# Performance work log

Hardware: AMD Instinct MI355X
Metric: run time of the kernel (lower is better)

## Reference

```python
import jax, jax.numpy as jnp
import numpy as np

B, S, H = 8, 2048, 1024
NEG = 1.0e10


def setup_inputs() -> dict:
    key = jax.random.key(0)
    ks = jax.random.split(key, 9)
    scale = 1.0 / np.sqrt(H)
    x = jax.random.normal(ks[0], (B, S, H), dtype=jnp.float32)
    Wq = jax.random.normal(ks[1], (H, H), dtype=jnp.float32) * scale
    bq = jnp.zeros((H,), dtype=jnp.float32)
    Wk = jax.random.normal(ks[2], (H, H), dtype=jnp.float32) * scale
    bk = jnp.zeros((H,), dtype=jnp.float32)
    Wv = jax.random.normal(ks[3], (H, H), dtype=jnp.float32) * scale
    bv = jnp.zeros((H,), dtype=jnp.float32)
    gamma = jnp.ones((H,), dtype=jnp.float32)
    beta = jnp.zeros((H,), dtype=jnp.float32)
    return {"x": x, "Wq": Wq, "bq": bq, "Wk": Wk, "bk": bk,
            "Wv": Wv, "bv": bv, "gamma": gamma, "beta": beta}


def _layernorm(y, gamma, beta, eps=1e-5):
    mu = jnp.mean(y, axis=-1, keepdims=True)
    var = jnp.var(y, axis=-1, keepdims=True)
    return (y - mu) * jax.lax.rsqrt(var + eps) * gamma + beta


def reference(x, Wq, bq, Wk, bk, Wv, bv, gamma, beta):
    # QKV projections (single head, no 1/sqrt(d) scaling, per original code)
    q = x @ Wq + bq                       # [B, S, H]
    k = x @ Wk + bk                       # [B, S, H]
    v = x @ Wv + bv                       # [B, S, H]
    scores = jnp.einsum('bsh,bth->bst', q, k)   # [B, S, S]
    # non-standard multiplicative-subtractive causal mask
    mask = jnp.tril(jnp.ones((S, S), dtype=scores.dtype))  # [S, S]
    scores = scores * mask - NEG * (1.0 - mask)
    probs = jax.nn.softmax(scores, axis=-1)
    attn = jnp.einsum('bst,bth->bsh', probs, v)
    return _layernorm(v + attn, gamma, beta)
```

## Files before the change

### kernel.cpp

```cpp
#include <hip/hip_runtime.h>

#define SQ 2048
#define HD 1024
#define NB 8
#define NT2 8
#define NTOT (NB*SQ)
#define CE ((long long)72*32768)

typedef _Float16 f16x8 __attribute__((ext_vector_type(8)));
typedef float f32x4 __attribute__((ext_vector_type(4)));
typedef short s16x8 __attribute__((ext_vector_type(8)));
typedef short s16x4 __attribute__((ext_vector_type(4)));
typedef unsigned short u16;

__device__ __forceinline__ u16 f2h(float x){
  _Float16 h = (_Float16)x;
  u16 u; __builtin_memcpy(&u, &h, 2); return u;
}

__device__ __forceinline__ int TB128(int i){
  int m = i >> 1;
  return (i & 1) ? (m + 1) * (m + 1) : m * m + m;
}

#define STG(gp, lp) __builtin_amdgcn_global_load_lds( \
    (const __attribute__((address_space(1))) unsigned*)(gp), \
    (__attribute__((address_space(3))) unsigned*)(lp), 16, 0, 0)

template<int EPI>
__global__ __launch_bounds__(512, 2)
void gemm8(const u16* __restrict__ A, const u16* __restrict__ B,
           float* Cf, u16* Ch, u16* Vt,
           const float* __restrict__ b0, const float* __restrict__ b1,
           const float* __restrict__ b2,
           int K, int lda, int ldb, int ldc,
           long long sA, long long sB, long long sC)
{
  const int z = blockIdx.z;
  const int bi = blockIdx.x, bj = blockIdx.y;

  __shared__ short lds[65536];

  const int tid  = threadIdx.x;
  const int lane = tid & 63, w = tid >> 6;
  const int wm2 = w >> 2, wn4 = w & 3;
  const int lrow = lane & 15, kgrp = lane >> 4;

  const long long rowA = (long long)bi * 256;
  const long long colB = (long long)bj * 256;

  const int rt = tid >> 3;
  const int gs = (tid & 7) ^ (rt & 7);

  const u16 *sAp[4], *sBp[4];
  if (EPI == 2){
    const u16* P0 = A + (long long)z * sA + (long long)(bi * bi + bi) * 65536;
    const u16* P1 = A + (long long)z * sA + (long long)((bi + 1) * (bi + 1)) * 65536;
    sAp[0] = P0 + (      rt) * 512 + gs * 8;
    sAp[1] = P0 + (64  + rt) * 512 + gs * 8;
    sAp[2] = P1 + (      rt) * 512 + gs * 8;
    sAp[3] = P1 + (64  + rt) * 512 + gs * 8;
  } else {
    const u16* Ab0 = A;
    #pragma unroll
    for (int i = 0; i < 4; i++)
      sAp[i] = Ab0 + (rowA + i * 64 + rt) * (long long)lda + gs * 8;
  }
  {
    const u16* Bb = B + (long long)z * sB;
    #pragma unroll
    for (int i = 0; i < 4; i++)
      sBp[i] = Bb + (colB + i * 64 + rt) * (long long)ldb + gs * 8;
  }

  #define ADST(buf,i) (lds + (buf) * 32768 +         (i) * 4096 + w * 512)
  #define BDST(buf,i) (lds + (buf) * 32768 + 16384 + (i) * 4096 + w * 512)

  const int fl = lrow & 7;
  const int swzk[2] = { ((0 + kgrp) ^ fl) * 8, ((4 + kgrp) ^ fl) * 8 };
  const int arow = (wm2 * 128 + lrow) * 64;
  const int brow = 16384 + (wn4 * 64 + lrow) * 64;

  f32x4 acc[8][4];
  const f32x4 zf = {0.f, 0.f, 0.f, 0.f};
  #pragma unroll
  for (int m = 0; m < 8; m++)
    #pragma unroll
    for (int n = 0; n < 4; n++) acc[m][n] = zf;

  int KT = K >> 6;
  if (EPI == 2){ int t = (bi + 1) * 4; if (t < KT) KT = t; }

  auto advance = [&](int tS){
    long long advA = 64;
    if (EPI == 2) advA = ((tS & 3) == 3) ? (65536 - 192) : 64;
    #pragma unroll
    for (int i = 0; i < 4; i++){ sAp[i] += advA; sBp[i] += 64; }
  };

  #pragma unroll
  for (int i = 0; i < 4; i++) STG(sAp[i], ADST(0, i));
  #pragma unroll
  for (int i = 0; i < 4; i++) STG(sBp[i], BDST(0, i));
  advance(0);
  __syncthreads();

  int cur = 0;
  for (int kt = 0; kt < KT; ++kt){
    const bool pf = (kt + 1 < KT);
    const short* Ab = lds + cur * 32768;
    const int nb = cur ^ 1;

    if (pf){
      #pragma unroll
      for (int i = 0; i < 4; i++) STG(sAp[i], ADST(nb, i));
      #pragma unroll
      for (int i = 0; i < 4; i++) STG(sBp[i], BDST(nb, i));
      advance(kt + 1);
    }

    f16x8 bq[4][2];
    #pragma unroll
    for (int n = 0; n < 4; n++)
      #pragma unroll
      for (int ks = 0; ks < 2; ks++)
        bq[n][ks] = *(const f16x8*)(Ab + brow + n * 1024 + swzk[ks]);

    #pragma unroll
    for (int qm = 0; qm < 2; qm++){
      f16x8 aq[4][2];
      #pragma unroll
      for (int m4 = 0; m4 < 4; m4++)
        #pragma unroll
        for (int ks = 0; ks < 2; ks++)
          aq[m4][ks] = *(const f16x8*)(Ab + arow + (qm * 4 + m4) * 1024 + swzk[ks]);

      __builtin_amdgcn_s_setprio(1);
      #pragma unroll
      for (int ks = 0; ks < 2; ks++)
        #pragma unroll
        for (int n = 0; n < 4; n++)
          #pragma unroll
          for (int m4 = 0; m4 < 4; m4++)
            acc[qm * 4 + m4][n] =
              __builtin_amdgcn_mfma_f32_16x16x32_f16(aq[m4][ks], bq[n][ks],
                                                     acc[qm * 4 + m4][n], 0, 0, 0);
      __builtin_amdgcn_s_setprio(0);
    }

    __syncthreads();
    cur ^= 1;
  }
  #undef ADST
  #undef BDST

  if (EPI == 0){
    if (z < 2){
      u16* c = Ch + (long long)z * sC;
      const float* bias = z ? b1 : b0;
      #pragma unroll
      for (int n = 0; n < 4; n++){
        int col = (int)colB + wn4 * 64 + n * 16 + lrow;
        float ba = bias[col];
        #pragma unroll
        for (int m = 0; m < 8; m++){
          long long r = rowA + wm2 * 128 + m * 16 + kgrp * 4;
          #pragma unroll
          for (int j = 0; j < 4; j++)
            c[(r + j) * ldc + col] = f2h(acc[m][n][j] + ba);
        }
      }
    } else {
      #pragma unroll
      for (int n = 0; n < 4; n++){
        int col = (int)colB + wn4 * 64 + n * 16 + lrow;
        float ba = b2[col];
        #pragma unroll
        for (int m = 0; m < 8; m++){
          long long r = rowA + wm2 * 128 + m * 16 + kgrp * 4;
          int bb = (int)(r >> 11);
          int s  = (int)(r & 2047);
          u16* vtc = Vt + ((long long)bb * HD + col) * SQ + s;
          #pragma unroll
          for (int j = 0; j < 4; j++){
            float v = acc[m][n][j] + ba;
            Cf[(r + j) * ldc + col] = v;
            vtc[j] = f2h(v);
          }
        }
      }
    }
  } else {
    float* cf = Cf + (long long)z * sC;
    #pragma unroll
    for (int n = 0; n < 4; n++){
      int col = (int)colB + wn4 * 64 + n * 16 + lrow;
      #pragma unroll
      for (int m = 0; m < 8; m++){
        long long r = rowA + wm2 * 128 + m * 16 + kgrp * 4;
        #pragma unroll
        for (int j = 0; j < 4; j++){
          long long o = (r + j) * ldc + col;
          cf[o] = acc[m][n][j] + cf[o];
        }
      }
    }
  }
}

__global__ __launch_bounds__(512, 2)
void gemm_sc(const u16* __restrict__ A, const u16* __restrict__ B,
             float* Cf, long long sA, long long sB, long long sC)
{
  const int z = blockIdx.z;
  int t = blockIdx.x;
  int i = (int)(2.f * sqrtf((float)t));
  if (i > 15) i = 15;
  while (TB128(i + 1) <= t) ++i;
  while (TB128(i) > t) --i;
  const int bj = t - TB128(i);

  __shared__ short lds[2 * 24576];

  const int tid  = threadIdx.x;
  const int lane = tid & 63, w = tid >> 6;
  const int wm2 = w >> 2, wn4 = w & 3;
  const int lrow = lane & 15, kgrp = lane >> 4;

  const long long rowA = (long long)i * 128;
  const long long colB = (long long)bj * 256;

  const int rt = tid >> 3;
  const int gs = (tid & 7) ^ (rt & 7);

  const u16 *sAp[2], *sBp[4];
  {
    const u16* Ab0 = A + (long long)z * sA;
    #pragma unroll
    for (int k = 0; k < 2; k++)
      sAp[k] = Ab0 + (rowA + k * 64 + rt) * (long long)HD + gs * 8;
    const u16* Bb = B + (long long)z * sB;
    #pragma unroll
    for (int k = 0; k < 4; k++)
      sBp[k] = Bb + (colB + k * 64 + rt) * (long long)HD + gs * 8;
  }

  #define ADST2(buf,k) (lds + (buf) * 24576 +        (k) * 4096 + w * 512)
  #define BDST2(buf,k) (lds + (buf) * 24576 + 8192 + (k) * 4096 + w * 512)

  const int fl = lrow & 7;
  const int swzk[2] = { ((0 + kgrp) ^ fl) * 8, ((4 + kgrp) ^ fl) * 8 };
  const int arow = (wm2 * 64 + lrow) * 64;
  const int brow = 8192 + (wn4 * 64 + lrow) * 64;

  f32x4 acc[4][4];
  const f32x4 zf = {0.f, 0.f, 0.f, 0.f};
  #pragma unroll
  for (int m = 0; m < 4; m++)
    #pragma unroll
    for (int n = 0; n < 4; n++) acc[m][n] = zf;

  const int KT = HD >> 6;

  auto advance = [&](){
    #pragma unroll
    for (int k = 0; k < 2; k++) sAp[k] += 64;
    #pragma unroll
    for (int k = 0; k < 4; k++) sBp[k] += 64;
  };

  #pragma unroll
  for (int k = 0; k < 2; k++) STG(sAp[k], ADST2(0, k));
  #pragma unroll
  for (int k = 0; k < 4; k++) STG(sBp[k], BDST2(0, k));
  advance();
  __syncthreads();

  int cur = 0;
  for (int kt = 0; kt < KT; ++kt){
    const bool pf = (kt + 1 < KT);
    const short* Ab = lds + cur * 24576;
    const int nb = cur ^ 1;

    if (pf){
      #pragma unroll
      for (int k = 0; k < 2; k++) STG(sAp[k], ADST2(nb, k));
      #pragma unroll
      for (int k = 0; k < 4; k++) STG(sBp[k], BDST2(nb, k));
      advance();
    }

    f16x8 bq[4][2], aq[4][2];
    #pragma unroll
    for (int n = 0; n < 4; n++)
      #pragma unroll
      for (int ks = 0; ks < 2; ks++)
        bq[n][ks] = *(const f16x8*)(Ab + brow + n * 1024 + swzk[ks]);
    #pragma unroll
    for (int m = 0; m < 4; m++)
      #pragma unroll
      for (int ks = 0; ks < 2; ks++)
        aq[m][ks] = *(const f16x8*)(Ab + arow + m * 1024 + swzk[ks]);

    __builtin_amdgcn_s_setprio(1);
    #pragma unroll
    for (int ks = 0; ks < 2; ks++)
      #pragma unroll
      for (int n = 0; n < 4; n++)
        #pragma unroll
        for (int m = 0; m < 4; m++)
          acc[m][n] = __builtin_amdgcn_mfma_f32_16x16x32_f16(aq[m][ks], bq[n][ks],
                                                             acc[m][n], 0, 0, 0);
    __builtin_amdgcn_s_setprio(0);

    __syncthreads();
    cur ^= 1;
  }
  #undef ADST2
  #undef BDST2

  float* cf = Cf + (long long)z * sC + (long long)t * 32768;
  #pragma unroll
  for (int n = 0; n < 4; n++){
    int col = wn4 * 64 + n * 16 + lrow;
    #pragma unroll
    for (int m = 0; m < 4; m++){
      int r = wm2 * 64 + m * 16 + kgrp * 4;
      #pragma unroll
      for (int j = 0; j < 4; j++)
        cf[(r + j) * 256 + col] = acc[m][n][j];
    }
  }
}

__global__ __launch_bounds__(256)
void prep_x(const float* __restrict__ X, u16* __restrict__ Xh)
{
  const long long n8 = (long long)NTOT * HD / 8;
  for (long long i = (long long)blockIdx.x * 256 + threadIdx.x; i < n8;
       i += (long long)gridDim.x * 256){
    const float* p = X + i * 8;
    float4 a = *(const float4*)p;
    float4 b = *(const float4*)(p + 4);
    float f[8] = {a.x, a.y, a.z, a.w, b.x, b.y, b.z, b.w};
    s16x8 h;
    #pragma unroll
    for (int j = 0; j < 8; j++) h[j] = (short)f2h(f[j]);
    *(s16x8*)&Xh[i * 8] = h;
  }
}

__global__ void prep_w(const float* __restrict__ Wq, const float* __restrict__ Wk,
                       const float* __restrict__ Wv, u16* __restrict__ Wt)
{
  __shared__ float t[32][33];
  const float* Win = (blockIdx.z == 0) ? Wq : (blockIdx.z == 1) ? Wk : Wv;
  const size_t zo = (size_t)blockIdx.z * HD * HD;
  int n0 = blockIdx.x * 32, k0 = blockIdx.y * 32;
  int tx = threadIdx.x, ty = threadIdx.y;
  #pragma unroll
  for (int i = 0; i < 4; i++)
    t[ty + 8*i][tx] = Win[(size_t)(k0 + ty + 8*i) * HD + n0 + tx];
  __syncthreads();
  #pragma unroll
  for (int i = 0; i < 4; i++)
    Wt[zo + (size_t)(n0 + ty + 8*i) * HD + k0 + tx] = f2h(t[tx][ty + 8*i]);
}

__global__ __launch_bounds__(256)
void softmax_causal(const float* __restrict__ SC, u16* __restrict__ P)
{
  const int s = blockIdx.x;
  const int ti = s >> 7;
  const int tb = TB128(ti);
  const float* scb = SC + (long long)blockIdx.y * CE + (long long)tb * 32768
                   + (long long)(s & 127) * 256;
  u16* pb = P + (long long)blockIdx.y * (2 * CE) + (long long)tb * 65536
          + (long long)(s & 127) * 512;

  __shared__ float buf[SQ];
  __shared__ float red[4];
  const int tid = threadIdx.x, lane = tid & 63, wid = tid >> 6;

  float m = -3.4e38f;
  const int nfull = (s + 1) & ~3;
  for (int t4 = tid * 4; t4 < nfull; t4 += 1024){
    float4 v = *(const float4*)&scb[(t4 >> 8) * 32768 + (t4 & 255)];
    *(float4*)&buf[t4] = v;
    m = fmaxf(fmaxf(fmaxf(m, v.x), v.y), fmaxf(v.z, v.w));
  }
  for (int t = nfull + tid; t <= s; t += 256){
    float v = scb[(t >> 8) * 32768 + (t & 255)];
    buf[t] = v; m = fmaxf(m, v);
  }
  #pragma unroll
  for (int o = 32; o; o >>= 1) m = fmaxf(m, __shfl_xor(m, o));
  if (lane == 0) red[wid] = m;
  __syncthreads();
  m = fmaxf(fmaxf(red[0], red[1]), fmaxf(red[2], red[3]));
  __syncthreads();

  float sum = 0.f;
  for (int t = tid; t <= s; t += 256){ float e = __expf(buf[t] - m); buf[t] = e; sum += e; }
  #pragma unroll
  for (int o = 32; o; o >>= 1) sum += __shfl_xor(sum, o);
  if (lane == 0) red[wid] = sum;
  __syncthreads();
  sum = red[0] + red[1] + red[2] + red[3];
  const float inv = 1.f / sum;

  const int lim = ((ti >> 1) + 1) << 8;
  for (int t4 = tid * 4; t4 < lim; t4 += 1024){
    s16x4 pk;
    #pragma unroll
    for (int j = 0; j < 4; j++){
      int t = t4 + j;
      pk[j] = (t <= s) ? (short)f2h(buf[t] * inv) : (short)0;
    }
    *(s16x4*)&pb[(t4 >> 8) * 65536 + (t4 & 255)] = pk;
  }
}

__global__ __launch_bounds__(256)
void layernorm_inplace(float* __restrict__ Y, const float* __restrict__ gamma,
                       const float* __restrict__ beta)
{
  float* y = Y + (long long)blockIdx.x * HD;
  const int tid = threadIdx.x, lane = tid & 63, wid = tid >> 6;
  float xv[4];
  float s = 0.f, ss = 0.f;
  #pragma unroll
  for (int i = 0; i < 4; i++){
    float v = y[tid + i * 256];
    xv[i] = v; s += v; ss += v * v;
  }
  #pragma unroll
  for (int o = 32; o; o >>= 1){ s += __shfl_xor(s, o); ss += __shfl_xor(ss, o); }
  __shared__ float r1[4], r2[4];
  if (lane == 0){ r1[wid] = s; r2[wid] = ss; }
  __syncthreads();
  s  = r1[0] + r1[1] + r1[2] + r1[3];
  ss = r2[0] + r2[1] + r2[2] + r2[3];
  const float mu   = s * (1.f / HD);
  const float var  = ss * (1.f / HD) - mu * mu;
  const float rstd = rsqrtf(var + 1e-5f);
  #pragma unroll
  for (int i = 0; i < 4; i++){
    int c = tid + i * 256;
    y[c] = (xv[i] - mu) * rstd * gamma[c] + beta[c];
  }
}

extern "C" void kernel_launch(void* const* d_in, const int* in_sizes, int n_in,
                              void* d_out, int out_size, void* d_ws, size_t ws_size,
                              hipStream_t stream)
{
  const float* x     = (const float*)d_in[0];
  const float* Wq    = (const float*)d_in[1];
  const float* bq    = (const float*)d_in[2];
  const float* Wk    = (const float*)d_in[3];
  const float* bk    = (const float*)d_in[4];
  const float* Wv    = (const float*)d_in[5];
  const float* bv    = (const float*)d_in[6];
  const float* gamma = (const float*)d_in[7];
  const float* beta  = (const float*)d_in[8];
  float* out = (float*)d_out;

  char* wsp = (char*)d_ws;
  size_t off = 0;
  auto alloc = [&](size_t bytes) -> char* {
    char* p = wsp + off;
    off = (off + bytes + 255) & ~(size_t)255;
    return p;
  };

  u16* Wt = (u16*)alloc(3ULL * HD * HD * 2);
  u16* QK = (u16*)alloc(2ULL * NTOT * HD * 2);
  u16* Vt = (u16*)alloc((size_t)NB * HD * SQ * 2);

  size_t rem = (ws_size > off) ? (ws_size - off) : 0;
  size_t perb = (size_t)CE * 4;
  int G = (int)(rem / perb);
  if (G > NB) G = NB;
  if (G < 1)  G = 1;
  u16*   xh = (u16*)(wsp + off);
  float* SC = (float*)(wsp + off);

  u16* Qh = QK;
  u16* Kh = QK + (size_t)NTOT * HD;
  float* V = out;

  prep_x<<<dim3(2048), dim3(256), 0, stream>>>(x, xh);
  prep_w<<<dim3(HD/32, HD/32, 3), dim3(32, 8), 0, stream>>>(Wq, Wk, Wv, Wt);

  gemm8<0><<<dim3(NTOT/256, HD/256, 3), 512, 0, stream>>>(
      xh, Wt, V, QK, Vt, bq, bk, bv,
      HD, HD, HD, HD,
      0LL, (long long)HD * HD, (long long)NTOT * HD);

  for (int g0 = 0; g0 < NB; g0 += G){
    int g = (G < NB - g0) ? G : (NB - g0);
    gemm_sc<<<dim3(72, 1, g), 512, 0, stream>>>(
        Qh + (size_t)g0 * SQ * HD, Kh + (size_t)g0 * SQ * HD, SC,
        (long long)SQ * HD, (long long)SQ * HD, CE);
    softmax_causal<<<dim3(SQ, g), 256, 0, stream>>>(SC, (u16*)SC);
    gemm8<2><<<dim3(NT2, HD/256, g), 512, 0, stream>>>(
        (const u16*)SC, Vt + (size_t)g0 * HD * SQ,
        out + (size_t)g0 * SQ * HD, nullptr, nullptr, nullptr, nullptr, nullptr,
        SQ, 512, SQ, HD,
        2 * CE, (long long)HD * SQ, (long long)SQ * HD);
  }

  layernorm_inplace<<<dim3(NTOT), 256, 0, stream>>>(out, gamma, beta);
}
```

Measured before the change: 332.9 us.

## Split causal PV GEMM into dedicated 128-row-tile kernel for better load balance

Measured after the change: 333.4 us. No clear change (+0.2%).

```diff
diff --git a/kernel.cpp b/kernel.cpp
--- a/kernel.cpp
+++ b/kernel.cpp
@@ -53,14 +53,7 @@
   const int gs = (tid & 7) ^ (rt & 7);
 
   const u16 *sAp[4], *sBp[4];
-  if (EPI == 2){
-    const u16* P0 = A + (long long)z * sA + (long long)(bi * bi + bi) * 65536;
-    const u16* P1 = A + (long long)z * sA + (long long)((bi + 1) * (bi + 1)) * 65536;
-    sAp[0] = P0 + (      rt) * 512 + gs * 8;
-    sAp[1] = P0 + (64  + rt) * 512 + gs * 8;
-    sAp[2] = P1 + (      rt) * 512 + gs * 8;
-    sAp[3] = P1 + (64  + rt) * 512 + gs * 8;
-  } else {
+  {
     const u16* Ab0 = A;
     #pragma unroll
     for (int i = 0; i < 4; i++)
@@ -88,21 +81,18 @@
     #pragma unroll
     for (int n = 0; n < 4; n++) acc[m][n] = zf;
 
-  int KT = K >> 6;
-  if (EPI == 2){ int t = (bi + 1) * 4; if (t < KT) KT = t; }
-
-  auto advance = [&](int tS){
-    long long advA = 64;
-    if (EPI == 2) advA = ((tS & 3) == 3) ? (65536 - 192) : 64;
-    #pragma unroll
-    for (int i = 0; i < 4; i++){ sAp[i] += advA; sBp[i] += 64; }
+  const int KT = K >> 6;
+
+  auto advance = [&](){
+    #pragma unroll
+    for (int i = 0; i < 4; i++){ sAp[i] += 64; sBp[i] += 64; }
   };
 
   #pragma unroll
   for (int i = 0; i < 4; i++) STG(sAp[i], ADST(0, i));
   #pragma unroll
   for (int i = 0; i < 4; i++) STG(sBp[i], BDST(0, i));
-  advance(0);
+  advance();
   __syncthreads();
 
   int cur = 0;
@@ -116,7 +106,7 @@
       for (int i = 0; i < 4; i++) STG(sAp[i], ADST(nb, i));
       #pragma unroll
       for (int i = 0; i < 4; i++) STG(sBp[i], BDST(nb, i));
-      advance(kt + 1);
+      advance();
     }
 
     f16x8 bq[4][2];
@@ -154,54 +144,37 @@
   #undef ADST
   #undef BDST
 
-  if (EPI == 0){
-    if (z < 2){
-      u16* c = Ch + (long long)z * sC;
-      const float* bias = z ? b1 : b0;
-      #pragma unroll
-      for (int n = 0; n < 4; n++){
-        int col = (int)colB + wn4 * 64 + n * 16 + lrow;
-        float ba = bias[col];
-        #pragma unroll
-        for (int m = 0; m < 8; m++){
-          long long r = rowA + wm2 * 128 + m * 16 + kgrp * 4;
-          #pragma unroll
-          for (int j = 0; j < 4; j++)
-            c[(r + j) * ldc + col] = f2h(acc[m][n][j] + ba);
-        }
-      }
-    } else {
-      #pragma unroll
-      for (int n = 0; n < 4; n++){
-        int col = (int)colB + wn4 * 64 + n * 16 + lrow;
-        float ba = b2[col];
-        #pragma unroll
-        for (int m = 0; m < 8; m++){
-          long long r = rowA + wm2 * 128 + m * 16 + kgrp * 4;
-          int bb = (int)(r >> 11);
-          int s  = (int)(r & 2047);
-          u16* vtc = Vt + ((long long)bb * HD + col) * SQ + s;
-          #pragma unroll
-          for (int j = 0; j < 4; j++){
-            float v = acc[m][n][j] + ba;
-            Cf[(r + j) * ldc + col] = v;
-            vtc[j] = f2h(v);
-          }
-        }
-      }
-    }
-  } else {
-    float* cf = Cf + (long long)z * sC;
+  if (z < 2){
+    u16* c = Ch + (long long)z * sC;
+    const float* bias = z ? b1 : b0;
     #pragma unroll
     for (int n = 0; n < 4; n++){
       int col = (int)colB + wn4 * 64 + n * 16 + lrow;
+      float ba = bias[col];
       #pragma unroll
       for (int m = 0; m < 8; m++){
         long long r = rowA + wm2 * 128 + m * 16 + kgrp * 4;
         #pragma unroll
+        for (int j = 0; j < 4; j++)
+          c[(r + j) * ldc + col] = f2h(acc[m][n][j] + ba);
+      }
+    }
+  } else {
+    #pragma unroll
+    for (int n = 0; n < 4; n++){
+      int col = (int)colB + wn4 * 64 + n * 16 + lrow;
+      float ba = b2[col];
+      #pragma unroll
+      for (int m = 0; m < 8; m++){
+        long long r = rowA + wm2 * 128 + m * 16 + kgrp * 4;
+        int bb = (int)(r >> 11);
+        int s  = (int)(r & 2047);
+        u16* vtc = Vt + ((long long)bb * HD + col) * SQ + s;
+        #pragma unroll
         for (int j = 0; j < 4; j++){
-          long long o = (r + j) * ldc + col;
-          cf[o] = acc[m][n][j] + cf[o];
+          float v = acc[m][n][j] + ba;
+          Cf[(r + j) * ldc + col] = v;
+          vtc[j] = f2h(v);
         }
       }
     }
@@ -329,6 +302,131 @@
       #pragma unroll
       for (int j = 0; j < 4; j++)
         cf[(r + j) * 256 + col] = acc[m][n][j];
+    }
+  }
+}
+
+__global__ __launch_bounds__(512, 2)
+void gemm_pv(const u16* __restrict__ P, const u16* __restrict__ Vt,
+             float* __restrict__ Out,
+             long long sP, long long sVt, long long sO)
+{
+  const int z = blockIdx.z;
+  const int ti = 15 - (int)blockIdx.x;
+  const int bj = blockIdx.y;
+  const int tb = TB128(ti);
+
+  __shared__ short lds[2 * 24576];
+
+  const int tid  = threadIdx.x;
+  const int lane = tid & 63, w = tid >> 6;
+  const int wm2 = w >> 2, wn4 = w & 3;
+  const int lrow = lane & 15, kgrp = lane >> 4;
+
+  const long long rowA = (long long)ti * 128;
+  const long long colB = (long long)bj * 256;
+
+  const int rt = tid >> 3;
+  const int gs = (tid & 7) ^ (rt & 7);
+
+  const u16 *sAp[2], *sBp[4];
+  {
+    const u16* Pb = P + (long long)z * sP + (long long)tb * 65536;
+    #pragma unroll
+    for (int k = 0; k < 2; k++)
+      sAp[k] = Pb + (k * 64 + rt) * 512 + gs * 8;
+    const u16* Bb = Vt + (long long)z * sVt;
+    #pragma unroll
+    for (int k = 0; k < 4; k++)
+      sBp[k] = Bb + (colB + k * 64 + rt) * (long long)SQ + gs * 8;
+  }
+
+  #define ADST3(buf,k) (lds + (buf) * 24576 +        (k) * 4096 + w * 512)
+  #define BDST3(buf,k) (lds + (buf) * 24576 + 8192 + (k) * 4096 + w * 512)
+
+  const int fl = lrow & 7;
+  const int swzk[2] = { ((0 + kgrp) ^ fl) * 8, ((4 + kgrp) ^ fl) * 8 };
+  const int arow = (wm2 * 64 + lrow) * 64;
+  const int brow = 8192 + (wn4 * 64 + lrow) * 64;
+
+  f32x4 acc[4][4];
+  const f32x4 zf = {0.f, 0.f, 0.f, 0.f};
+  #pragma unroll
+  for (int m = 0; m < 4; m++)
+    #pragma unroll
+    for (int n = 0; n < 4; n++) acc[m][n] = zf;
+
+  const int KT = ((ti >> 1) + 1) * 4;
+
+  auto advance = [&](int tS){
+    long long advA = ((tS & 3) == 3) ? (65536 - 192) : 64;
+    sAp[0] += advA; sAp[1] += advA;
+    #pragma unroll
+    for (int k = 0; k < 4; k++) sBp[k] += 64;
+  };
+
+  #pragma unroll
+  for (int k = 0; k < 2; k++) STG(sAp[k], ADST3(0, k));
+  #pragma unroll
+  for (int k = 0; k < 4; k++) STG(sBp[k], BDST3(0, k));
+  advance(0);
+  __syncthreads();
+
+  int cur = 0;
+  for (int kt = 0; kt < KT; ++kt){
+    const bool pf = (kt + 1 < KT);
+    const short* Ab = lds + cur * 24576;
+    const int nb = cur ^ 1;
+
+    if (pf){
+      #pragma unroll
+      for (int k = 0; k < 2; k++) STG(sAp[k], ADST3(nb, k));
+      #pragma unroll
+      for (int k = 0; k < 4; k++) STG(sBp[k], BDST3(nb, k));
+      advance(kt + 1);
+    }
+
+    f16x8 bq[4][2], aq[4][2];
+    #pragma unroll
+    for (int n = 0; n < 4; n++)
+      #pragma unroll
+      for (int ks = 0; ks < 2; ks++)
+        bq[n][ks] = *(const f16x8*)(Ab + brow + n * 1024 + swzk[ks]);
+    #pragma unroll
+    for (int m = 0; m < 4; m++)
+      #pragma unroll
+      for (int ks = 0; ks < 2; ks++)
+        aq[m][ks] = *(const f16x8*)(Ab + arow + m * 1024 + swzk[ks]);
+
+    __builtin_amdgcn_s_setprio(1);
+    #pragma unroll
+    for (int ks = 0; ks < 2; ks++)
+      #pragma unroll
+      for (int n = 0; n < 4; n++)
+        #pragma unroll
+        for (int m = 0; m < 4; m++)
+          acc[m][n] = __builtin_amdgcn_mfma_f32_16x16x32_f16(aq[m][ks], bq[n][ks],
+                                                             acc[m][n], 0, 0, 0);
+    __builtin_amdgcn_s_setprio(0);
+
+    __syncthreads();
+    cur ^= 1;
+  }
+  #undef ADST3
+  #undef BDST3
+
+  float* of = Out + (long long)z * sO;
+  #pragma unroll
+  for (int n = 0; n < 4; n++){
+    int col = (int)colB + wn4 * 64 + n * 16 + lrow;
+    #pragma unroll
+    for (int m = 0; m < 4; m++){
+      long long r = rowA + wm2 * 64 + m * 16 + kgrp * 4;
+      #pragma unroll
+      for (int j = 0; j < 4; j++){
+        long long o = (r + j) * HD + col;
+        of[o] = acc[m][n][j] + of[o];
+      }
     }
   }
 }
@@ -504,10 +602,9 @@
         Qh + (size_t)g0 * SQ * HD, Kh + (size_t)g0 * SQ * HD, SC,
         (long long)SQ * HD, (long long)SQ * HD, CE);
     softmax_causal<<<dim3(SQ, g), 256, 0, stream>>>(SC, (u16*)SC);
-    gemm8<2><<<dim3(NT2, HD/256, g), 512, 0, stream>>>(
+    gemm_pv<<<dim3(16, HD/256, g), 512, 0, stream>>>(
         (const u16*)SC, Vt + (size_t)g0 * HD * SQ,
-        out + (size_t)g0 * SQ * HD, nullptr, nullptr, nullptr, nullptr, nullptr,
-        SQ, 512, SQ, HD,
+        out + (size_t)g0 * SQ * HD,
         2 * CE, (long long)HD * SQ, (long long)SQ * HD);
   }
 
```
